# Kernel optimization log

Hardware: AMD Instinct MI355X
Metric: run time of the kernel (lower is better)

Reference implementation:

```python
import jax, jax.numpy as jnp
import numpy as np

THRESHOLD = 1.0
TAU_H, TAU_O = 50.0, 30.0

def setup_inputs() -> dict:
    key = jax.random.key(0)
    k1, k2, k3, k4, k5, k6 = jax.random.split(key, 6)
    B, T, S, H = 2048, 1024, 64, 256
    return {
        "sensor_history": jax.random.uniform(k1, (B, T, S), dtype=jnp.float32),
        "noise": jax.random.uniform(k2, (B, T, S), dtype=jnp.float32),
        "W_h": jax.random.normal(k3, (H, S), dtype=jnp.float32) * (1.0 / np.sqrt(S)),
        "b_h": jax.random.normal(k4, (H,), dtype=jnp.float32) * 0.01,
        "W_o": jax.random.normal(k5, (1, H), dtype=jnp.float32) * (1.0 / np.sqrt(H)),
        "b_o": jax.random.normal(k6, (1,), dtype=jnp.float32) * 0.01,
    }

def reference(sensor_history, noise, W_h, b_h, W_o, b_o):
    B, T, S = sensor_history.shape
    beta_h = jnp.exp(jnp.float32(-1.0 / TAU_H))  # membrane decay, hidden
    beta_o = jnp.exp(jnp.float32(-1.0 / TAU_O))  # membrane decay, output

    def step(carry, xs):
        v_h, v_o, acc = carry
        sensor_t, noise_t = xs  # (B, S) each
        # stochastic rate coding: spike if uniform < sensor value
        spikes_in = (noise_t < sensor_t).astype(jnp.float32)
        # hidden LIF: leaky integrate, threshold, hard reset
        v_h = beta_h * v_h + spikes_in @ W_h.T + b_h
        s_h = (v_h >= THRESHOLD).astype(jnp.float32)
        v_h = v_h * (1.0 - s_h)
        # output LIF
        v_o = beta_o * v_o + s_h @ W_o.T + b_o
        s_o = (v_o >= THRESHOLD).astype(jnp.float32)
        v_o = v_o * (1.0 - s_o)
        return (v_h, v_o, acc + s_o), None

    v_h0 = jnp.zeros((B, W_h.shape[0]), dtype=jnp.float32)
    v_o0 = jnp.zeros((B, 1), dtype=jnp.float32)
    acc0 = jnp.zeros((B, 1), dtype=jnp.float32)
    # time-major scan over the recurrence
    xs = (jnp.swapaxes(sensor_history, 0, 1), jnp.swapaxes(noise, 0, 1))
    (_, _, acc), _ = jax.lax.scan(step, (v_h0, v_o0, acc0), xs)
    return acc / jnp.float32(T)
```

## Files before the change

kernel.cpp:

```cpp
#include <hip/hip_runtime.h>

#define TT 1024
#define SS 64
#define HH 256
#define BB 4
#define TC 16
#define NC (TT / TC)

typedef _Float16 f16x8 __attribute__((ext_vector_type(8)));
typedef float    f32x4 __attribute__((ext_vector_type(4)));
typedef unsigned int u32x4 __attribute__((ext_vector_type(4)));

__device__ __forceinline__ void lgkm_barrier() {
    asm volatile("s_waitcnt lgkmcnt(0)" ::: "memory");
    __builtin_amdgcn_s_barrier();
}

template <int CTRL>
__device__ __forceinline__ float dpp_add(float x) {
    int v = __float_as_int(x);
    int m = __builtin_amdgcn_update_dpp(v, v, CTRL, 0xF, 0xF, true);
    return x + __int_as_float(m);
}
__device__ __forceinline__ float wxsum_row(float x) {
    x = dpp_add<0x124>(x);
    x = dpp_add<0x128>(x);
    return x;
}

__device__ __forceinline__ void rowsum16_x4(float& a, float& b, float& c, float& d) {
    asm volatile(
        "v_add_f32_dpp %0, %0, %0 quad_perm:[1,0,3,2] row_mask:0xf bank_mask:0xf\n\t"
        "v_add_f32_dpp %1, %1, %1 quad_perm:[1,0,3,2] row_mask:0xf bank_mask:0xf\n\t"
        "v_add_f32_dpp %2, %2, %2 quad_perm:[1,0,3,2] row_mask:0xf bank_mask:0xf\n\t"
        "v_add_f32_dpp %3, %3, %3 quad_perm:[1,0,3,2] row_mask:0xf bank_mask:0xf\n\t"
        "v_add_f32_dpp %0, %0, %0 quad_perm:[2,3,0,1] row_mask:0xf bank_mask:0xf\n\t"
        "v_add_f32_dpp %1, %1, %1 quad_perm:[2,3,0,1] row_mask:0xf bank_mask:0xf\n\t"
        "v_add_f32_dpp %2, %2, %2 quad_perm:[2,3,0,1] row_mask:0xf bank_mask:0xf\n\t"
        "v_add_f32_dpp %3, %3, %3 quad_perm:[2,3,0,1] row_mask:0xf bank_mask:0xf\n\t"
        "v_add_f32_dpp %0, %0, %0 row_half_mirror row_mask:0xf bank_mask:0xf\n\t"
        "v_add_f32_dpp %1, %1, %1 row_half_mirror row_mask:0xf bank_mask:0xf\n\t"
        "v_add_f32_dpp %2, %2, %2 row_half_mirror row_mask:0xf bank_mask:0xf\n\t"
        "v_add_f32_dpp %3, %3, %3 row_half_mirror row_mask:0xf bank_mask:0xf\n\t"
        "v_add_f32_dpp %0, %0, %0 row_mirror row_mask:0xf bank_mask:0xf\n\t"
        "v_add_f32_dpp %1, %1, %1 row_mirror row_mask:0xf bank_mask:0xf\n\t"
        "v_add_f32_dpp %2, %2, %2 row_mirror row_mask:0xf bank_mask:0xf\n\t"
        "v_add_f32_dpp %3, %3, %3 row_mirror row_mask:0xf bank_mask:0xf"
        : "+v"(a), "+v"(b), "+v"(c), "+v"(d));
}

__launch_bounds__(512, 4)
__global__ void snn_fused(const float* __restrict__ sensor,
                          const float* __restrict__ noise,
                          const float* __restrict__ Wh,
                          const float* __restrict__ bh,
                          const float* __restrict__ Wo,
                          const float* __restrict__ bo,
                          float* __restrict__ out)
{
    __shared__ __align__(16) char  spk[2][4 * 16 * 128];
    __shared__ __align__(16) float rpart[2][BB][8][TC];

    const int tid  = threadIdx.x;
    const int lane = tid & 63;
    const int wave = tid >> 6;
    const int b0   = blockIdx.x * BB;

    f16x8 whi[2][2], wlo[2][2];
    #pragma unroll
    for (int nti = 0; nti < 2; ++nti) {
        const int h = (wave + nti * 8) * 16 + (lane & 15);
        #pragma unroll
        for (int kh = 0; kh < 2; ++kh) {
            const int k = kh * 32 + (lane >> 4) * 8;
            const float* p = Wh + (size_t)h * SS + k;
            float4 wa = *(const float4*)(p);
            float4 wb = *(const float4*)(p + 4);
            float wv[8] = {wa.x, wa.y, wa.z, wa.w, wb.x, wb.y, wb.z, wb.w};
            f16x8 fh, fl;
            #pragma unroll
            for (int j = 0; j < 8; ++j) {
                _Float16 hi = (_Float16)wv[j];
                float r1 = wv[j] - (float)hi;
                fh[j] = hi;
                fl[j] = (_Float16)(r1 * 2048.0f);
            }
            whi[nti][kh] = fh; wlo[nti][kh] = fl;
        }
    }

    const int hc = lane & 15;
    const float bh0 = bh[wave * 16 + hc], bh1 = bh[128 + wave * 16 + hc];
    const float wo0 = Wo[wave * 16 + hc], wo1 = Wo[128 + wave * 16 + hc];
    const float bov = bo[0];
    const float betah = expf(-1.0f / 50.0f);
    const float betao = expf(-1.0f / 30.0f);

    const f32x4 zero4 = {0.0f, 0.0f, 0.0f, 0.0f};

    float vh0 = 0.0f, vh1 = 0.0f;
    float vo = 0.0f, acc = 0.0f;

    const int wtw  = tid >> 7;
    const int wm   = (tid >> 3) & 15;
    const int woct = tid & 7;
    const int wrow = wtw * 16 + wm;
    const int wbyte = wrow * 128 + ((woct * 16) ^ ((wrow & 7) << 4));
    const float* sgp = sensor + ((size_t)(b0 + (wm >> 2)) * TT + wtw * 4 + (wm & 3)) * SS + woct * 8;
    const float* ngp = noise  + ((size_t)(b0 + (wm >> 2)) * TT + wtw * 4 + (wm & 3)) * SS + woct * 8;

    float4 sA, sB, nA, nB;

    auto pack_spk = [&](char* dst) {
        u32x4 sv;
        sv[0] = (nA.x < sA.x ? 0x3C00u : 0u) | (nA.y < sA.y ? 0x3C000000u : 0u);
        sv[1] = (nA.z < sA.z ? 0x3C00u : 0u) | (nA.w < sA.w ? 0x3C000000u : 0u);
        sv[2] = (nB.x < sB.x ? 0x3C00u : 0u) | (nB.y < sB.y ? 0x3C000000u : 0u);
        sv[3] = (nB.z < sB.z ? 0x3C00u : 0u) | (nB.w < sB.w ? 0x3C000000u : 0u);
        *(u32x4*)(dst + wbyte) = sv;
    };

    auto p4_step = [&](const float (*rp)[TC]) {
        const int wx  = (lane >> 2) & 7;
        const int twq = lane & 3;
        float4 q = *(const float4*)&rp[wx][twq * 4];
        q.x = wxsum_row(q.x); q.x += __shfl_xor(q.x, 16);
        q.y = wxsum_row(q.y); q.y += __shfl_xor(q.y, 16);
        q.z = wxsum_row(q.z); q.z += __shfl_xor(q.z, 16);
        q.w = wxsum_row(q.w); q.w += __shfl_xor(q.w, 16);
        #pragma unroll
        for (int ph = 0; ph < 4; ++ph) {
            if ((lane & 3) == ph) {
                float so;
                vo = (betao * vo + q.x) + bov; so = (vo >= 1.0f) ? 1.0f : 0.0f; vo = (vo >= 1.0f) ? 0.0f : vo; acc += so;
                vo = (betao * vo + q.y) + bov; so = (vo >= 1.0f) ? 1.0f : 0.0f; vo = (vo >= 1.0f) ? 0.0f : vo; acc += so;
                vo = (betao * vo + q.z) + bov; so = (vo >= 1.0f) ? 1.0f : 0.0f; vo = (vo >= 1.0f) ? 0.0f : vo; acc += so;
                vo = (betao * vo + q.w) + bov; so = (vo >= 1.0f) ? 1.0f : 0.0f; vo = (vo >= 1.0f) ? 0.0f : vo; acc += so;
            }
            vo  = __shfl(vo, ph);
            acc = __shfl(acc, ph);
        }
    };

    sA = *(const float4*)(sgp);     sB = *(const float4*)(sgp + 4);
    nA = *(const float4*)(ngp);     nB = *(const float4*)(ngp + 4);
    pack_spk(spk[0]);
    {
        const float* ps = sgp + (size_t)1 * TC * SS;
        const float* pn = ngp + (size_t)1 * TC * SS;
        sA = *(const float4*)(ps);  sB = *(const float4*)(ps + 4);
        nA = *(const float4*)(pn);  nB = *(const float4*)(pn + 4);
    }
    lgkm_barrier();

    const int abase = hc * 128;
    const int koff0 = (((lane >> 4)    ) * 16) ^ ((hc & 7) << 4);
    const int koff1 = (((lane >> 4) + 4) * 16) ^ ((hc & 7) << 4);

    for (int c = 0; c < NC; ++c) {
        const int cur = c & 1;

        if (c + 1 < NC) pack_spk(spk[cur ^ 1]);

        if (c + 2 < NC) {
            const float* ps = sgp + (size_t)(c + 2) * TC * SS;
            const float* pn = ngp + (size_t)(c + 2) * TC * SS;
            sA = *(const float4*)(ps);  sB = *(const float4*)(ps + 4);
            nA = *(const float4*)(pn);  nB = *(const float4*)(pn + 4);
        }

        if (c > 0 && wave < 4) p4_step(rpart[cur ^ 1][wave]);

        const char* sp = spk[cur];
        f16x8 a0 = *(const f16x8*)(sp + abase + koff0);
        f16x8 a1 = *(const f16x8*)(sp + abase + koff1);
        #pragma unroll
        for (int tw = 0; tw < 4; ++tw) {
            f16x8 n0, n1;
            if (tw < 3) {
                const char* np = sp + abase + (tw + 1) * 2048;
                n0 = *(const f16x8*)(np + koff0);
                n1 = *(const f16x8*)(np + koff1);
            } else { n0 = a0; n1 = a1; }

            f32x4 ah0 = __builtin_amdgcn_mfma_f32_16x16x32_f16(a0, whi[0][0], zero4, 0, 0, 0);
            ah0       = __builtin_amdgcn_mfma_f32_16x16x32_f16(a1, whi[0][1], ah0,   0, 0, 0);
            f32x4 al0 = __builtin_amdgcn_mfma_f32_16x16x32_f16(a0, wlo[0][0], zero4, 0, 0, 0);
            al0       = __builtin_amdgcn_mfma_f32_16x16x32_f16(a1, wlo[0][1], al0,   0, 0, 0);
            f32x4 ah1 = __builtin_amdgcn_mfma_f32_16x16x32_f16(a0, whi[1][0], zero4, 0, 0, 0);
            ah1       = __builtin_amdgcn_mfma_f32_16x16x32_f16(a1, whi[1][1], ah1,   0, 0, 0);
            f32x4 al1 = __builtin_amdgcn_mfma_f32_16x16x32_f16(a0, wlo[1][0], zero4, 0, 0, 0);
            al1       = __builtin_amdgcn_mfma_f32_16x16x32_f16(a1, wlo[1][1], al1,   0, 0, 0);

            float rr[4];
            #pragma unroll
            for (int r = 0; r < 4; ++r) {
                const float d0 = __builtin_fmaf(al0[r], 0x1p-11f, ah0[r]);
                const float d1 = __builtin_fmaf(al1[r], 0x1p-11f, ah1[r]);
                vh0 = __builtin_fmaf(betah, vh0, d0) + bh0;
                vh1 = __builtin_fmaf(betah, vh1, d1) + bh1;
                const bool c0 = (vh0 >= 1.0f);
                const bool c1 = (vh1 >= 1.0f);
                rr[r] = (c0 ? wo0 : 0.0f) + (c1 ? wo1 : 0.0f);
                vh0 = c0 ? 0.0f : vh0;
                vh1 = c1 ? 0.0f : vh1;
            }
            rowsum16_x4(rr[0], rr[1], rr[2], rr[3]);

            if (hc == 0) {
                float4 rq = make_float4(rr[0], rr[1], rr[2], rr[3]);
                *(float4*)&rpart[cur][lane >> 4][wave][tw * 4] = rq;
            }
            a0 = n0; a1 = n1;
        }

        lgkm_barrier();
    }

    if (wave < 4) {
        p4_step(rpart[(NC - 1) & 1][wave]);
        if (lane == 0) out[b0 + wave] = acc * (1.0f / (float)TT);
    }
}

extern "C" void kernel_launch(void* const* d_in, const int* in_sizes, int n_in,
                              void* d_out, int out_size, void* d_ws, size_t ws_size,
                              hipStream_t stream)
{
    const float* sensor = (const float*)d_in[0];
    const float* noise  = (const float*)d_in[1];
    const float* Wh     = (const float*)d_in[2];
    const float* bh     = (const float*)d_in[3];
    const float* Wo     = (const float*)d_in[4];
    const float* bo     = (const float*)d_in[5];
    float* out = (float*)d_out;

    const int B = in_sizes[0] / (TT * SS);
    dim3 grid(B / BB), block(512);
    hipLaunchKernelGGL(snn_fused, grid, block, 0, stream,
                       sensor, noise, Wh, bh, Wo, bo, out);
}
```

Measured before the change: 244.8 us.

## Split output LIF recurrence into a separate kernel via workspace buffer

The hidden-layer kernel no longer runs the serial output-neuron recurrence inside its chunk loop. Each chunk's per-timestep output current is reduced across waves (one rotating wave per chunk) and written to a global workspace. A second small kernel then runs the output LIF scan per batch element. This takes the serial DPP reduction and shuffle-heavy scan off the critical path of the main loop, at the cost of an extra launch and an 8 MB workspace round-trip. The fused version is kept as a fallback when the workspace is too small.

```diff
diff --git a/kernel.cpp b/kernel.cpp
--- a/kernel.cpp
+++ b/kernel.cpp
@@ -50,16 +50,15 @@
 }
 
 __launch_bounds__(512, 4)
-__global__ void snn_fused(const float* __restrict__ sensor,
-                          const float* __restrict__ noise,
-                          const float* __restrict__ Wh,
-                          const float* __restrict__ bh,
-                          const float* __restrict__ Wo,
-                          const float* __restrict__ bo,
-                          float* __restrict__ out)
+__global__ void snn_hidden(const float* __restrict__ sensor,
+                           const float* __restrict__ noise,
+                           const float* __restrict__ Wh,
+                           const float* __restrict__ bh,
+                           const float* __restrict__ Wo,
+                           float* __restrict__ rsum)
 {
     __shared__ __align__(16) char  spk[2][4 * 16 * 128];
-    __shared__ __align__(16) float rpart[2][BB][8][TC];
+    __shared__ __align__(16) float rpart[2][8][BB][TC];
 
     const int tid  = threadIdx.x;
     const int lane = tid & 63;
@@ -92,14 +91,10 @@
     const int hc = lane & 15;
     const float bh0 = bh[wave * 16 + hc], bh1 = bh[128 + wave * 16 + hc];
     const float wo0 = Wo[wave * 16 + hc], wo1 = Wo[128 + wave * 16 + hc];
-    const float bov = bo[0];
     const float betah = expf(-1.0f / 50.0f);
-    const float betao = expf(-1.0f / 30.0f);
-
     const f32x4 zero4 = {0.0f, 0.0f, 0.0f, 0.0f};
 
     float vh0 = 0.0f, vh1 = 0.0f;
-    float vo = 0.0f, acc = 0.0f;
 
     const int wtw  = tid >> 7;
     const int wm   = (tid >> 3) & 15;
@@ -120,26 +115,13 @@
         *(u32x4*)(dst + wbyte) = sv;
     };
 
-    auto p4_step = [&](const float (*rp)[TC]) {
-        const int wx  = (lane >> 2) & 7;
-        const int twq = lane & 3;
-        float4 q = *(const float4*)&rp[wx][twq * 4];
-        q.x = wxsum_row(q.x); q.x += __shfl_xor(q.x, 16);
-        q.y = wxsum_row(q.y); q.y += __shfl_xor(q.y, 16);
-        q.z = wxsum_row(q.z); q.z += __shfl_xor(q.z, 16);
-        q.w = wxsum_row(q.w); q.w += __shfl_xor(q.w, 16);
-        #pragma unroll
-        for (int ph = 0; ph < 4; ++ph) {
-            if ((lane & 3) == ph) {
-                float so;
-                vo = (betao * vo + q.x) + bov; so = (vo >= 1.0f) ? 1.0f : 0.0f; vo = (vo >= 1.0f) ? 0.0f : vo; acc += so;
-                vo = (betao * vo + q.y) + bov; so = (vo >= 1.0f) ? 1.0f : 0.0f; vo = (vo >= 1.0f) ? 0.0f : vo; acc += so;
-                vo = (betao * vo + q.z) + bov; so = (vo >= 1.0f) ? 1.0f : 0.0f; vo = (vo >= 1.0f) ? 0.0f : vo; acc += so;
-                vo = (betao * vo + q.w) + bov; so = (vo >= 1.0f) ? 1.0f : 0.0f; vo = (vo >= 1.0f) ? 0.0f : vo; acc += so;
-            }
-            vo  = __shfl(vo, ph);
-            acc = __shfl(acc, ph);
-        }
+    auto reduce_store = [&](int cprev) {
+        const float* rp = &rpart[cprev & 1][0][0][0];
+        const int rb = lane >> 4, rt = lane & 15;
+        float s = rp[rb * TC + rt];
+        #pragma unroll
+        for (int w = 1; w < 8; ++w) s += rp[w * (BB * TC) + rb * TC + rt];
+        rsum[(size_t)(b0 + rb) * TT + cprev * TC + rt] = s;
     };
 
     sA = *(const float4*)(sgp);     sB = *(const float4*)(sgp + 4);
@@ -169,7 +151,7 @@
             nA = *(const float4*)(pn);  nB = *(const float4*)(pn + 4);
         }
 
-        if (c > 0 && wave < 4) p4_step(rpart[cur ^ 1][wave]);
+        if (c > 0 && wave == (c & 7)) reduce_store(c - 1);
 
         const char* sp = spk[cur];
         f16x8 a0 = *(const f16x8*)(sp + abase + koff0);
@@ -209,11 +191,198 @@
 
             if (hc == 0) {
                 float4 rq = make_float4(rr[0], rr[1], rr[2], rr[3]);
+                *(float4*)&rpart[cur][wave][lane >> 4][tw * 4] = rq;
+            }
+            a0 = n0; a1 = n1;
+        }
+
+        lgkm_barrier();
+    }
+
+    if (wave == 0) reduce_store(NC - 1);
+}
+
+__launch_bounds__(256, 1)
+__global__ void snn_out(const float* __restrict__ rsum,
+                        const float* __restrict__ bo,
+                        float* __restrict__ out, int B)
+{
+    const int b = blockIdx.x * blockDim.x + threadIdx.x;
+    if (b >= B) return;
+    const float bov = bo[0];
+    const float betao = expf(-1.0f / 30.0f);
+    const float* rp = rsum + (size_t)b * TT;
+    float vo = 0.0f, acc = 0.0f;
+    for (int t = 0; t < TT; t += 4) {
+        float4 q = *(const float4*)(rp + t);
+        float so;
+        vo = (betao * vo + q.x) + bov; so = (vo >= 1.0f) ? 1.0f : 0.0f; vo = (vo >= 1.0f) ? 0.0f : vo; acc += so;
+        vo = (betao * vo + q.y) + bov; so = (vo >= 1.0f) ? 1.0f : 0.0f; vo = (vo >= 1.0f) ? 0.0f : vo; acc += so;
+        vo = (betao * vo + q.z) + bov; so = (vo >= 1.0f) ? 1.0f : 0.0f; vo = (vo >= 1.0f) ? 0.0f : vo; acc += so;
+        vo = (betao * vo + q.w) + bov; so = (vo >= 1.0f) ? 1.0f : 0.0f; vo = (vo >= 1.0f) ? 0.0f : vo; acc += so;
+    }
+    out[b] = acc * (1.0f / (float)TT);
+}
+
+__launch_bounds__(512, 4)
+__global__ void snn_mono(const float* __restrict__ sensor,
+                         const float* __restrict__ noise,
+                         const float* __restrict__ Wh,
+                         const float* __restrict__ bh,
+                         const float* __restrict__ Wo,
+                         const float* __restrict__ bo,
+                         float* __restrict__ out)
+{
+    __shared__ __align__(16) char  spk[2][4 * 16 * 128];
+    __shared__ __align__(16) float rpart[2][BB][8][TC];
+
+    const int tid  = threadIdx.x;
+    const int lane = tid & 63;
+    const int wave = tid >> 6;
+    const int b0   = blockIdx.x * BB;
+
+    f16x8 whi[2][2], wlo[2][2];
+    #pragma unroll
+    for (int nti = 0; nti < 2; ++nti) {
+        const int h = (wave + nti * 8) * 16 + (lane & 15);
+        #pragma unroll
+        for (int kh = 0; kh < 2; ++kh) {
+            const int k = kh * 32 + (lane >> 4) * 8;
+            const float* p = Wh + (size_t)h * SS + k;
+            float4 wa = *(const float4*)(p);
+            float4 wb = *(const float4*)(p + 4);
+            float wv[8] = {wa.x, wa.y, wa.z, wa.w, wb.x, wb.y, wb.z, wb.w};
+            f16x8 fh, fl;
+            #pragma unroll
+            for (int j = 0; j < 8; ++j) {
+                _Float16 hi = (_Float16)wv[j];
+                float r1 = wv[j] - (float)hi;
+                fh[j] = hi;
+                fl[j] = (_Float16)(r1 * 2048.0f);
+            }
+            whi[nti][kh] = fh; wlo[nti][kh] = fl;
+        }
+    }
+
+    const int hc = lane & 15;
+    const float bh0 = bh[wave * 16 + hc], bh1 = bh[128 + wave * 16 + hc];
+    const float wo0 = Wo[wave * 16 + hc], wo1 = Wo[128 + wave * 16 + hc];
+    const float bov = bo[0];
+    const float betah = expf(-1.0f / 50.0f);
+    const float betao = expf(-1.0f / 30.0f);
+    const f32x4 zero4 = {0.0f, 0.0f, 0.0f, 0.0f};
+
+    float vh0 = 0.0f, vh1 = 0.0f;
+    float vo = 0.0f, acc = 0.0f;
+
+    const int wtw  = tid >> 7;
+    const int wm   = (tid >> 3) & 15;
+    const int woct = tid & 7;
+    const int wrow = wtw * 16 + wm;
+    const int wbyte = wrow * 128 + ((woct * 16) ^ ((wrow & 7) << 4));
+    const float* sgp = sensor + ((size_t)(b0 + (wm >> 2)) * TT + wtw * 4 + (wm & 3)) * SS + woct * 8;
+    const float* ngp = noise  + ((size_t)(b0 + (wm >> 2)) * TT + wtw * 4 + (wm & 3)) * SS + woct * 8;
+
+    float4 sA, sB, nA, nB;
+
+    auto pack_spk = [&](char* dst) {
+        u32x4 sv;
+        sv[0] = (nA.x < sA.x ? 0x3C00u : 0u) | (nA.y < sA.y ? 0x3C000000u : 0u);
+        sv[1] = (nA.z < sA.z ? 0x3C00u : 0u) | (nA.w < sA.w ? 0x3C000000u : 0u);
+        sv[2] = (nB.x < sB.x ? 0x3C00u : 0u) | (nB.y < sB.y ? 0x3C000000u : 0u);
+        sv[3] = (nB.z < sB.z ? 0x3C00u : 0u) | (nB.w < sB.w ? 0x3C000000u : 0u);
+        *(u32x4*)(dst + wbyte) = sv;
+    };
+
+    auto p4_step = [&](const float (*rp)[TC]) {
+        const int wx  = (lane >> 2) & 7;
+        const int twq = lane & 3;
+        float4 q = *(const float4*)&rp[wx][twq * 4];
+        q.x = wxsum_row(q.x); q.x += __shfl_xor(q.x, 16);
+        q.y = wxsum_row(q.y); q.y += __shfl_xor(q.y, 16);
+        q.z = wxsum_row(q.z); q.z += __shfl_xor(q.z, 16);
+        q.w = wxsum_row(q.w); q.w += __shfl_xor(q.w, 16);
+        #pragma unroll
+        for (int ph = 0; ph < 4; ++ph) {
+            if ((lane & 3) == ph) {
+                float so;
+                vo = (betao * vo + q.x) + bov; so = (vo >= 1.0f) ? 1.0f : 0.0f; vo = (vo >= 1.0f) ? 0.0f : vo; acc += so;
+                vo = (betao * vo + q.y) + bov; so = (vo >= 1.0f) ? 1.0f : 0.0f; vo = (vo >= 1.0f) ? 0.0f : vo; acc += so;
+                vo = (betao * vo + q.z) + bov; so = (vo >= 1.0f) ? 1.0f : 0.0f; vo = (vo >= 1.0f) ? 0.0f : vo; acc += so;
+                vo = (betao * vo + q.w) + bov; so = (vo >= 1.0f) ? 1.0f : 0.0f; vo = (vo >= 1.0f) ? 0.0f : vo; acc += so;
+            }
+            vo  = __shfl(vo, ph);
+            acc = __shfl(acc, ph);
+        }
+    };
+
+    sA = *(const float4*)(sgp);     sB = *(const float4*)(sgp + 4);
+    nA = *(const float4*)(ngp);     nB = *(const float4*)(ngp + 4);
+    pack_spk(spk[0]);
+    {
+        const float* ps = sgp + (size_t)1 * TC * SS;
+        const float* pn = ngp + (size_t)1 * TC * SS;
+        sA = *(const float4*)(ps);  sB = *(const float4*)(ps + 4);
+        nA = *(const float4*)(pn);  nB = *(const float4*)(pn + 4);
+    }
+    lgkm_barrier();
+
+    const int abase = hc * 128;
+    const int koff0 = (((lane >> 4)    ) * 16) ^ ((hc & 7) << 4);
+    const int koff1 = (((lane >> 4) + 4) * 16) ^ ((hc & 7) << 4);
+
+    for (int c = 0; c < NC; ++c) {
+        const int cur = c & 1;
+        if (c + 1 < NC) pack_spk(spk[cur ^ 1]);
+        if (c + 2 < NC) {
+            const float* ps = sgp + (size_t)(c + 2) * TC * SS;
+            const float* pn = ngp + (size_t)(c + 2) * TC * SS;
+            sA = *(const float4*)(ps);  sB = *(const float4*)(ps + 4);
+            nA = *(const float4*)(pn);  nB = *(const float4*)(pn + 4);
+        }
+        if (c > 0 && wave < 4) p4_step(rpart[cur ^ 1][wave]);
+
+        const char* sp = spk[cur];
+        f16x8 a0 = *(const f16x8*)(sp + abase + koff0);
+        f16x8 a1 = *(const f16x8*)(sp + abase + koff1);
+        #pragma unroll
+        for (int tw = 0; tw < 4; ++tw) {
+            f16x8 n0, n1;
+            if (tw < 3) {
+                const char* np = sp + abase + (tw + 1) * 2048;
+                n0 = *(const f16x8*)(np + koff0);
+                n1 = *(const f16x8*)(np + koff1);
+            } else { n0 = a0; n1 = a1; }
+
+            f32x4 ah0 = __builtin_amdgcn_mfma_f32_16x16x32_f16(a0, whi[0][0], zero4, 0, 0, 0);
+            ah0       = __builtin_amdgcn_mfma_f32_16x16x32_f16(a1, whi[0][1], ah0,   0, 0, 0);
+            f32x4 al0 = __builtin_amdgcn_mfma_f32_16x16x32_f16(a0, wlo[0][0], zero4, 0, 0, 0);
+            al0       = __builtin_amdgcn_mfma_f32_16x16x32_f16(a1, wlo[0][1], al0,   0, 0, 0);
+            f32x4 ah1 = __builtin_amdgcn_mfma_f32_16x16x32_f16(a0, whi[1][0], zero4, 0, 0, 0);
+            ah1       = __builtin_amdgcn_mfma_f32_16x16x32_f16(a1, whi[1][1], ah1,   0, 0, 0);
+            f32x4 al1 = __builtin_amdgcn_mfma_f32_16x16x32_f16(a0, wlo[1][0], zero4, 0, 0, 0);
+            al1       = __builtin_amdgcn_mfma_f32_16x16x32_f16(a1, wlo[1][1], al1,   0, 0, 0);
+
+            float rr[4];
+            #pragma unroll
+            for (int r = 0; r < 4; ++r) {
+                const float d0 = __builtin_fmaf(al0[r], 0x1p-11f, ah0[r]);
+                const float d1 = __builtin_fmaf(al1[r], 0x1p-11f, ah1[r]);
+                vh0 = __builtin_fmaf(betah, vh0, d0) + bh0;
+                vh1 = __builtin_fmaf(betah, vh1, d1) + bh1;
+                const bool c0 = (vh0 >= 1.0f);
+                const bool c1 = (vh1 >= 1.0f);
+                rr[r] = (c0 ? wo0 : 0.0f) + (c1 ? wo1 : 0.0f);
+                vh0 = c0 ? 0.0f : vh0;
+                vh1 = c1 ? 0.0f : vh1;
+            }
+            rowsum16_x4(rr[0], rr[1], rr[2], rr[3]);
+            if (hc == 0) {
+                float4 rq = make_float4(rr[0], rr[1], rr[2], rr[3]);
                 *(float4*)&rpart[cur][lane >> 4][wave][tw * 4] = rq;
             }
             a0 = n0; a1 = n1;
         }
-
         lgkm_barrier();
     }
 
@@ -236,7 +405,19 @@
     float* out = (float*)d_out;
 
     const int B = in_sizes[0] / (TT * SS);
-    dim3 grid(B / BB), block(512);
-    hipLaunchKernelGGL(snn_fused, grid, block, 0, stream,
-                       sensor, noise, Wh, bh, Wo, bo, out);
-}
+    const size_t need = (size_t)B * TT * sizeof(float);
+
+    if (ws_size >= need) {
+        float* rsum = (float*)d_ws;
+        dim3 grid1(B / BB), block1(512);
+        hipLaunchKernelGGL(snn_hidden, grid1, block1, 0, stream,
+                           sensor, noise, Wh, bh, Wo, rsum);
+        dim3 grid2((B + 255) / 256), block2(256);
+        hipLaunchKernelGGL(snn_out, grid2, block2, 0, stream,
+                           rsum, bo, out, B);
+    } else {
+        dim3 grid(B / BB), block(512);
+        hipLaunchKernelGGL(snn_mono, grid, block, 0, stream,
+                           sensor, noise, Wh, bh, Wo, bo, out);
+    }
+}
```

After: 298.5 us. 1.22x slower.
